# Optimization experiments

Hardware: AMD Instinct MI355X
Metric: run time of the kernel (lower is better)

## Reference

```python
import jax, jax.numpy as jnp
import numpy as np

N = 100000
E = 1600000
D_IN = 64
D_HID = 64
D_OUT = 40
BN_EPS = 1e-5


def setup_inputs() -> dict:
    key = jax.random.key(0)
    ks = jax.random.split(key, 8)
    x = jax.random.normal(ks[0], (N, D_IN), dtype=jnp.float32)
    edge_index = jax.random.randint(ks[1], (2, E), 0, N, dtype=jnp.int64)
    # SAGEConv params: out = lin_l(aggr_neigh) + lin_r(x); bias lives in lin_l
    s1 = 1.0 / np.sqrt(D_IN)
    W1l = jax.random.uniform(ks[2], (D_HID, D_IN), jnp.float32, -s1, s1)
    W1r = jax.random.uniform(ks[3], (D_HID, D_IN), jnp.float32, -s1, s1)
    b1 = jnp.zeros((D_HID,), jnp.float32)
    gamma = jnp.ones((D_HID,), jnp.float32)
    beta = jnp.zeros((D_HID,), jnp.float32)
    s2 = 1.0 / np.sqrt(D_HID)
    W2l = jax.random.uniform(ks[4], (D_OUT, D_HID), jnp.float32, -s2, s2)
    W2r = jax.random.uniform(ks[5], (D_OUT, D_HID), jnp.float32, -s2, s2)
    b2 = jnp.zeros((D_OUT,), jnp.float32)
    return {"x": x, "edge_index": edge_index, "W1l": W1l, "W1r": W1r, "b1": b1,
            "gamma": gamma, "beta": beta, "W2l": W2l, "W2r": W2r, "b2": b2}


def _scatter_mean(feat, src, dst, n):
    # gather source-node features, scatter-mean onto destination nodes
    summed = jax.ops.segment_sum(feat[src], dst, num_segments=n)  # [N, D]
    cnt = jax.ops.segment_sum(jnp.ones((src.shape[0],), feat.dtype), dst, num_segments=n)
    return summed / jnp.maximum(cnt, 1.0)[:, None]


def _sage_conv(h, src, dst, Wl, Wr, b):
    agg = _scatter_mean(h, src, dst, h.shape[0])
    return agg @ Wl.T + h @ Wr.T + b


def reference(x, edge_index, W1l, W1r, b1, gamma, beta, W2l, W2r, b2):
    src, dst = edge_index[0], edge_index[1]
    h = _sage_conv(x, src, dst, W1l, W1r, b1)
    # BatchNorm1d (training-mode batch statistics, biased variance)
    mu = jnp.mean(h, axis=0)
    var = jnp.mean(jnp.square(h - mu), axis=0)
    h = (h - mu) * jax.lax.rsqrt(var + BN_EPS) * gamma + beta
    h = jax.nn.relu(h)
    # dropout is identity in eval mode
    out = _sage_conv(h, src, dst, W2l, W2r, b2)
    return out
```

## Files before the change

### kernel.cpp

```cpp
#include <hip/hip_runtime.h>
#include <hip/hip_fp8.h>

#define N_NODES 100000
#define N_EDGES 1600000
#define BN_EPS 1e-5f
#define E4 400000
#define CAP 64
#define NBINS 391
#define BINCAP 4608
#define BIN_MASK 255
#define G_BLOCKS 6250
#define NCOPY 32
#define D1B 391

typedef float v2f __attribute__((ext_vector_type(2)));
typedef __attribute__((ext_vector_type(8))) short bf16x8;
typedef __attribute__((ext_vector_type(4))) float f32x4;

__device__ __forceinline__ float bcast(float v, int k) {
    return __uint_as_float(__builtin_amdgcn_readlane(__float_as_uint(v), k));
}
__device__ __forceinline__ unsigned short f2bf(float x) {
    unsigned int u = __float_as_uint(x);
    return (unsigned short)((u + 0x7FFF + ((u >> 16) & 1)) >> 16);
}
__device__ __forceinline__ bf16x8 pack8(float4 a, float4 b) {
    bf16x8 r;
    r[0] = (short)f2bf(a.x); r[1] = (short)f2bf(a.y);
    r[2] = (short)f2bf(a.z); r[3] = (short)f2bf(a.w);
    r[4] = (short)f2bf(b.x); r[5] = (short)f2bf(b.y);
    r[6] = (short)f2bf(b.z); r[7] = (short)f2bf(b.w);
    return r;
}
__device__ __forceinline__ unsigned char f2fp8(float x) {
    return (unsigned char)__hip_cvt_float_to_fp8(x, __HIP_SATFINITE, __HIP_E4M3);
}
template <bool HI>
__device__ __forceinline__ v2f fp8x2(unsigned int w) {
#if __has_builtin(__builtin_amdgcn_cvt_pk_f32_fp8)
    return __builtin_amdgcn_cvt_pk_f32_fp8((int)w, HI);
#else
    unsigned int b = HI ? (w >> 16) : w;
    __half_raw h0 = __hip_cvt_fp8_to_halfraw((__hip_fp8_storage_t)(b & 0xFF), __HIP_E4M3);
    __half_raw h1 = __hip_cvt_fp8_to_halfraw((__hip_fp8_storage_t)((b >> 8) & 0xFF), __HIP_E4M3);
    v2f r; r.x = __half2float(__half(h0)); r.y = __half2float(__half(h1));
    return r;
#endif
}

__global__ __launch_bounds__(1024) void binA_kernel(
    const int4* __restrict__ src4, const int4* __restrict__ dst4,
    int* __restrict__ bcur, unsigned int* __restrict__ binbuf)
{
    __shared__ int lcnt[NBINS];
    __shared__ int lbase[NBINS];
    int tid = threadIdx.x;
    if (tid < NBINS) lcnt[tid] = 0;
    __syncthreads();

    int i = blockIdx.x * 1024 + tid;
    int4 d, s;
    int b0 = 0, b1 = 0, b2 = 0, b3 = 0, r0 = 0, r1 = 0, r2 = 0, r3 = 0;
    bool valid = (i < E4);
    if (valid) {
        d = dst4[i]; s = src4[i];
        b0 = d.x >> 8; r0 = atomicAdd(&lcnt[b0], 1);
        b1 = d.y >> 8; r1 = atomicAdd(&lcnt[b1], 1);
        b2 = d.z >> 8; r2 = atomicAdd(&lcnt[b2], 1);
        b3 = d.w >> 8; r3 = atomicAdd(&lcnt[b3], 1);
    }
    __syncthreads();
    if (tid < NBINS && lcnt[tid] > 0)
        lbase[tid] = atomicAdd(&bcur[tid], lcnt[tid]);
    __syncthreads();
    if (valid) {
        int p;
        p = lbase[b0] + r0; if (p < BINCAP) binbuf[(size_t)b0 * BINCAP + p] = ((unsigned)s.x << 8) | (unsigned)(d.x & BIN_MASK);
        p = lbase[b1] + r1; if (p < BINCAP) binbuf[(size_t)b1 * BINCAP + p] = ((unsigned)s.y << 8) | (unsigned)(d.y & BIN_MASK);
        p = lbase[b2] + r2; if (p < BINCAP) binbuf[(size_t)b2 * BINCAP + p] = ((unsigned)s.z << 8) | (unsigned)(d.z & BIN_MASK);
        p = lbase[b3] + r3; if (p < BINCAP) binbuf[(size_t)b3 * BINCAP + p] = ((unsigned)s.w << 8) | (unsigned)(d.w & BIN_MASK);
    }
}

__global__ __launch_bounds__(256) void binB_dense1_kernel(
    const unsigned int* __restrict__ binbuf, const int* __restrict__ bcur,
    int* __restrict__ cnt, int* __restrict__ nbrf,
    const float* __restrict__ x, const float* __restrict__ W1l,
    const float* __restrict__ W1r, const float* __restrict__ b1,
    unsigned char* __restrict__ u8, float* __restrict__ hv)
{
    if (blockIdx.x < NBINS) {
        __shared__ int lc[256];
        int tid = threadIdx.x;
        lc[tid] = 0;
        __syncthreads();
        int bin = blockIdx.x;
        int n = min(bcur[bin], BINCAP);
        for (int i = tid; i < n; i += 256) {
            unsigned int e = binbuf[(size_t)bin * BINCAP + i];
            int dl  = (int)(e & BIN_MASK);
            int src = (int)(e >> 8);
            int slot = atomicAdd(&lc[dl], 1);
            if (slot < CAP)
                nbrf[((size_t)(bin * 256 + dl)) * CAP + slot] = src;
        }
        __syncthreads();
        int node = bin * 256 + tid;
        if (node < N_NODES) {
            int c = min(lc[tid], CAP);
            cnt[node] = c;
            if (c == 0) nbrf[(size_t)node * CAP] = 0;
        }
        return;
    }

    int lane = threadIdx.x & 63;
    int wv   = threadIdx.x >> 6;
    int lr   = lane & 15;
    int lk   = lane >> 4;

    bf16x8 Bf[2][4][2];
#pragma unroll
    for (int mat = 0; mat < 2; ++mat) {
        const float* W = mat ? W1r : W1l;
#pragma unroll
        for (int ft = 0; ft < 4; ++ft) {
#pragma unroll
            for (int kh = 0; kh < 2; ++kh) {
                const float* p = W + (size_t)(ft * 16 + lr) * 64 + kh * 32 + lk * 8;
                Bf[mat][ft][kh] = pack8(*(const float4*)p, *(const float4*)(p + 4));
            }
        }
    }
    float b1v[4];
#pragma unroll
    for (int ft = 0; ft < 4; ++ft) b1v[ft] = b1[ft * 16 + lr];

    int nb = (blockIdx.x - NBINS) * 256;

    for (int it = 0; it < 4; ++it) {
        int n0 = nb + it * 64 + wv * 16;
        int arow = min(n0 + lr, N_NODES - 1);
        const float* xp = x + (size_t)arow * 64 + lk * 8;
        bf16x8 a0 = pack8(*(const float4*)xp,        *(const float4*)(xp + 4));
        bf16x8 a1 = pack8(*(const float4*)(xp + 32), *(const float4*)(xp + 36));

#pragma unroll
        for (int ft = 0; ft < 4; ++ft) {
            f32x4 Cl = {0.f, 0.f, 0.f, 0.f};
            f32x4 Cr = {0.f, 0.f, 0.f, 0.f};
            Cl = __builtin_amdgcn_mfma_f32_16x16x32_bf16(a0, Bf[0][ft][0], Cl, 0, 0, 0);
            Cl = __builtin_amdgcn_mfma_f32_16x16x32_bf16(a1, Bf[0][ft][1], Cl, 0, 0, 0);
            Cr = __builtin_amdgcn_mfma_f32_16x16x32_bf16(a0, Bf[1][ft][0], Cr, 0, 0, 0);
            Cr = __builtin_amdgcn_mfma_f32_16x16x32_bf16(a1, Bf[1][ft][1], Cr, 0, 0, 0);
#pragma unroll
            for (int r = 0; r < 4; ++r) {
                int node = n0 + lk * 4 + r;
                if (node < N_NODES) {
                    u8[(size_t)node * 64 + ft * 16 + lr] = f2fp8(Cl[r]);
                    hv[(size_t)node * 64 + ft * 16 + lr] = Cr[r] + b1v[ft];
                }
            }
        }
    }
}

__global__ __launch_bounds__(256) void gather1_bn_kernel(
    const unsigned short* __restrict__ u16, const int* __restrict__ cnt,
    const int* __restrict__ nbrf, float* __restrict__ hv,
    float* __restrict__ sumsR)
{
    __shared__ int sdeg[16];
    int node0 = blockIdx.x * 16;
    if (threadIdx.x < 16) {
        int n = node0 + threadIdx.x;
        sdeg[threadIdx.x] = (n < N_NODES) ? min(cnt[n], CAP) : 0;
    }
    __syncthreads();

    int lane = threadIdx.x & 63;
    int m    = lane & 31;
    int half = lane >> 5;
    int wv   = threadIdx.x >> 6;
    float s1_0 = 0.f, s1_1 = 0.f, s2_0 = 0.f, s2_1 = 0.f;

    int d0  = sdeg[wv];
    int idn = nbrf[(size_t)min(node0 + wv, N_NODES - 1) * CAP + min(lane, max(d0, 1) - 1)];

    for (int nn = 0; nn < 4; ++nn) {
        int li   = nn * 4 + wv;
        int node = node0 + li;
        int deg  = sdeg[li];
        int id   = idn;

        if (nn < 3) {
            int lin = li + 4;
            int dn  = sdeg[lin];
            idn = nbrf[(size_t)min(node0 + lin, N_NODES - 1) * CAP + min(lane, max(dn, 1) - 1)];
        }

        if (node < N_NODES) {
            float2 v = make_float2(0.f, 0.f);
            if (half == 0)
                v = ((const float2*)hv)[(size_t)node * 32 + m];

            float p0=0,p1=0,p2=0,p3=0,q0=0,q1=0,q2=0,q3=0;
            for (int r = 0; r < deg; r += 16) {
#pragma unroll
                for (int i = 0; i < 8; ++i) {
                    int e   = r + 2 * i + half;
                    int ide = __shfl(id, e);
                    unsigned int w = u16[(size_t)ide * 32 + m];
                    w = (e < deg) ? w : 0u;
                    v2f d = fp8x2<false>(w);
                    if ((i & 3) == 0)      { p0 += d.x; q0 += d.y; }
                    else if ((i & 3) == 1) { p1 += d.x; q1 += d.y; }
                    else if ((i & 3) == 2) { p2 += d.x; q2 += d.y; }
                    else                   { p3 += d.x; q3 += d.y; }
                }
            }
            float P = (p0 + p1) + (p2 + p3);
            float Q = (q0 + q1) + (q2 + q3);
            P += __shfl_xor(P, 32);
            Q += __shfl_xor(Q, 32);
            if (half == 0) {
                float inv = 1.0f / (float)max(deg, 1);
                float h0 = P * inv + v.x;
                float h1 = Q * inv + v.y;
                ((float2*)hv)[(size_t)node * 32 + m] = make_float2(h0, h1);
                s1_0 += h0; s1_1 += h1;
                s2_0 += h0 * h0; s2_1 += h1 * h1;
            }
        }
    }

    __shared__ float2 redA[256];
    __shared__ float2 redB[256];
    redA[threadIdx.x] = make_float2(s1_0, s1_1);
    redB[threadIdx.x] = make_float2(s2_0, s2_1);
    __syncthreads();
    if (threadIdx.x < 32) {
        int mm = threadIdx.x;
        float a0=0,a1=0,b0=0,b1=0;
        for (int w = 0; w < 4; ++w) {
            float2 A = redA[w * 64 + mm]; a0 += A.x; a1 += A.y;
            float2 B = redB[w * 64 + mm]; b0 += B.x; b1 += B.y;
        }
        float* base = sumsR + (size_t)(blockIdx.x & (NCOPY - 1)) * 128;
        atomicAdd(&base[2 * mm], a0);       atomicAdd(&base[2 * mm + 1], a1);
        atomicAdd(&base[64 + 2 * mm], b0);  atomicAdd(&base[64 + 2 * mm + 1], b1);
    }
}

__global__ __launch_bounds__(256) void dense2_bn_kernel(
    const float* __restrict__ h, const float* __restrict__ sumsR,
    const float* __restrict__ gamma, const float* __restrict__ beta,
    const float* __restrict__ W2l, const float* __restrict__ W2r,
    const float* __restrict__ b2,
    unsigned char* __restrict__ t40, float* __restrict__ out)
{
    __shared__ float wlT[64 * 65];
    __shared__ float wrT[64 * 65];
    for (int idx = threadIdx.x; idx < 2560; idx += 256) {
        int f = idx >> 6, k = idx & 63;
        wlT[k * 65 + f] = W2l[idx];
        wrT[k * 65 + f] = W2r[idx];
    }
    __syncthreads();

    int f  = threadIdx.x & 63;
    int wv = threadIdx.x >> 6;
    int fc = (f < 40) ? f : 39;
    float wl[64], wr[64];
#pragma unroll
    for (int k = 0; k < 64; ++k) {
        wl[k] = wlT[k * 65 + fc];
        wr[k] = wrT[k * 65 + fc];
    }
    float bias = b2[fc];

    float s = 0.f, q = 0.f;
#pragma unroll
    for (int c = 0; c < NCOPY; ++c) {
        s += sumsR[c * 128 + f];
        q += sumsR[c * 128 + 64 + f];
    }
    float inv_n = 1.0f / (float)N_NODES;
    float mu  = s * inv_n;
    float var = q * inv_n - mu * mu;
    float rs  = rsqrtf(var + BN_EPS);
    float sc  = gamma[f] * rs;
    float sh  = beta[f] - mu * sc;

    int node0 = blockIdx.x * 64;

    for (int nn = 0; nn < 16; ++nn) {
        int node = node0 + nn * 4 + wv;
        if (node < N_NODES) {
            float hvv = h[(size_t)node * 64 + f];
            float hn  = fmaxf(hvv * sc + sh, 0.f);
            float ta = 0.f, ra = bias;
#pragma unroll
            for (int k = 0; k < 64; ++k) {
                float hb = bcast(hn, k);
                ta += hb * wl[k];
                ra += hb * wr[k];
            }
            if (f < 40) {
                t40[(size_t)node * 64 + f] = f2fp8(ta);
                out[(size_t)node * 40 + f] = ra;
            }
        }
    }
}

__global__ __launch_bounds__(256) void gather2_kernel(
    const unsigned int* __restrict__ t40, const int* __restrict__ cnt,
    const int* __restrict__ nbrf, float* __restrict__ out)
{
    __shared__ int sdeg[16];
    int node0 = blockIdx.x * 16;
    if (threadIdx.x < 16) {
        int n = node0 + threadIdx.x;
        sdeg[threadIdx.x] = (n < N_NODES) ? min(cnt[n], CAP) : 0;
    }
    __syncthreads();

    int lane = threadIdx.x & 63;
    int q    = lane >> 4;
    int m    = lane & 15;
    int cl   = (m < 10) ? m : 9;
    int wv   = threadIdx.x >> 6;

    int dA = sdeg[wv], dB = sdeg[wv + 4];
    int idA = nbrf[(size_t)min(node0 + wv,     N_NODES - 1) * CAP + min(lane, max(dA, 1) - 1)];
    int idB = nbrf[(size_t)min(node0 + wv + 4, N_NODES - 1) * CAP + min(lane, max(dB, 1) - 1)];

    unsigned int r0A[4], r1A[4], r0B[4], r1B[4];
    {
        int cnt0 = dA;
#pragma unroll
        for (int i = 0; i < 4; ++i) {
            int e   = 4 * i + q;
            int ide = __shfl(idA, max(min(e, cnt0 - 1), 0));
            r0A[i] = t40[(size_t)ide * 16 + cl];
        }
        if (cnt0 > 16) {
#pragma unroll
            for (int i = 0; i < 4; ++i) {
                int e   = 16 + 4 * i + q;
                int ide = __shfl(idA, min(e, cnt0 - 1));
                r1A[i] = t40[(size_t)ide * 16 + cl];
            }
        }
    }

    for (int nn = 0; nn < 4; ++nn) {
        int li   = nn * 4 + wv;
        int node = node0 + li;
        int deg  = sdeg[li];

        int idC = 0;
        if (nn < 2) {
            int lic = li + 8;
            int dc  = sdeg[lic];
            idC = nbrf[(size_t)min(node0 + lic, N_NODES - 1) * CAP + min(lane, max(dc, 1) - 1)];
        }
        if (nn < 3) {
            int cntn = sdeg[li + 4];
#pragma unroll
            for (int i = 0; i < 4; ++i) {
                int e   = 4 * i + q;
                int ide = __shfl(idB, max(min(e, cntn - 1), 0));
                r0B[i] = t40[(size_t)ide * 16 + cl];
            }
            if (cntn > 16) {
#pragma unroll
                for (int i = 0; i < 4; ++i) {
                    int e   = 16 + 4 * i + q;
                    int ide = __shfl(idB, min(e, cntn - 1));
                    r1B[i] = t40[(size_t)ide * 16 + cl];
                }
            }
        }

        if (node < N_NODES) {
            float4 o = make_float4(0.f, 0.f, 0.f, 0.f);
            if (lane < 10)
                o = ((const float4*)out)[(size_t)node * 10 + m];

            float a0=0,a1=0,a2=0,a3=0, b0=0,b1=0,b2=0,b3=0;
#pragma unroll
            for (int i = 0; i < 4; ++i) {
                int e = 4 * i + q;
                unsigned int w = (e < deg) ? r0A[i] : 0u;
                v2f dlo = fp8x2<false>(w);
                v2f dhi = fp8x2<true>(w);
                if (i & 1) { b0 += dlo.x; b1 += dlo.y; b2 += dhi.x; b3 += dhi.y; }
                else       { a0 += dlo.x; a1 += dlo.y; a2 += dhi.x; a3 += dhi.y; }
            }
            if (deg > 16) {
#pragma unroll
                for (int i = 0; i < 4; ++i) {
                    int e = 16 + 4 * i + q;
                    unsigned int w = (e < deg) ? r1A[i] : 0u;
                    v2f dlo = fp8x2<false>(w);
                    v2f dhi = fp8x2<true>(w);
                    if (i & 1) { b0 += dlo.x; b1 += dlo.y; b2 += dhi.x; b3 += dhi.y; }
                    else       { a0 += dlo.x; a1 += dlo.y; a2 += dhi.x; a3 += dhi.y; }
                }
                for (int r = 32; r < deg; r += 16) {
#pragma unroll
                    for (int i = 0; i < 4; ++i) {
                        int e   = r + 4 * i + q;
                        int ide = __shfl(idA, min(e, deg - 1));
                        unsigned int w = t40[(size_t)ide * 16 + cl];
                        w = (e < deg) ? w : 0u;
                        v2f dlo = fp8x2<false>(w);
                        v2f dhi = fp8x2<true>(w);
                        if (i & 1) { b0 += dlo.x; b1 += dlo.y; b2 += dhi.x; b3 += dhi.y; }
                        else       { a0 += dlo.x; a1 += dlo.y; a2 += dhi.x; a3 += dhi.y; }
                    }
                }
            }
            a0 += b0; a1 += b1; a2 += b2; a3 += b3;
            a0 += __shfl_xor(a0, 16); a0 += __shfl_xor(a0, 32);
            a1 += __shfl_xor(a1, 16); a1 += __shfl_xor(a1, 32);
            a2 += __shfl_xor(a2, 16); a2 += __shfl_xor(a2, 32);
            a3 += __shfl_xor(a3, 16); a3 += __shfl_xor(a3, 32);
            if (lane < 10) {
                float inv = 1.0f / (float)max(deg, 1);
                o.x += a0 * inv;
                o.y += a1 * inv;
                o.z += a2 * inv;
                o.w += a3 * inv;
                ((float4*)out)[(size_t)node * 10 + m] = o;
            }
        }

        idA = idB; idB = idC;
#pragma unroll
        for (int i = 0; i < 4; ++i) { r0A[i] = r0B[i]; r1A[i] = r1B[i]; }
    }
}

extern "C" void kernel_launch(void* const* d_in, const int* in_sizes, int n_in,
                              void* d_out, int out_size, void* d_ws, size_t ws_size,
                              hipStream_t stream)
{
    const float* x     = (const float*)d_in[0];
    const int*   ei    = (const int*)d_in[1];
    const float* W1l   = (const float*)d_in[2];
    const float* W1r   = (const float*)d_in[3];
    const float* b1    = (const float*)d_in[4];
    const float* gamma = (const float*)d_in[5];
    const float* beta  = (const float*)d_in[6];
    const float* W2l   = (const float*)d_in[7];
    const float* W2r   = (const float*)d_in[8];
    const float* b2    = (const float*)d_in[9];
    float* out = (float*)d_out;

    const int4* src4 = (const int4*)ei;
    const int4* dst4 = (const int4*)(ei + N_EDGES);

    float* ws    = (float*)d_ws;
    float* hv    = ws;
    float* sumsR = hv + (size_t)N_NODES * 64;
    int* bcur = (int*)(sumsR + NCOPY * 128);
    int* cnt  = bcur + 392;
    int* nbrf = cnt + N_NODES;
    unsigned char* u8 = (unsigned char*)(nbrf + (size_t)N_NODES * 64);
    unsigned char* t40 = u8;
    unsigned int* binbuf = (unsigned int*)d_out;

    dim3 blk(256);

    (void)hipMemsetAsync(sumsR, 0, (size_t)(NCOPY * 128 + 392) * 4, stream);

    int dblocks = (N_NODES + 63) / 64;

    binA_kernel<<<391, 1024, 0, stream>>>(src4, dst4, bcur, binbuf);

    binB_dense1_kernel<<<NBINS + D1B, blk, 0, stream>>>(
        binbuf, bcur, cnt, nbrf, x, W1l, W1r, b1, u8, hv);

    gather1_bn_kernel<<<G_BLOCKS, blk, 0, stream>>>(
        (const unsigned short*)u8, cnt, nbrf, hv, sumsR);

    dense2_bn_kernel<<<dblocks, blk, 0, stream>>>(
        hv, sumsR, gamma, beta, W2l, W2r, b2, t40, out);
    gather2_kernel<<<G_BLOCKS, blk, 0, stream>>>(
        (const unsigned int*)t40, cnt, nbrf, out);
}
```

Measured before the change: 265.0 us.

## Compute second-layer dense transform with bf16 MFMA instead of scalar FMA loops

Replaces the per-lane readlane-broadcast scalar FMA matmul in the BN+dense2 kernel with bf16 16x16x32 MFMA instructions, keeping the weights in registers as bf16 fragments. BN scale and shift are computed once per block into shared memory, and each block now processes 256 nodes with 391 blocks. The goal is to remove the heavy VALU and readlane cost of the 64x40 matmuls. In exchange, activations and weights are rounded to bf16 before the products, which lowers precision, and the output stores become strided per MFMA row layout.

Result: faster. 225.2 us (-15.0%).

```diff
diff --git a/kernel.cpp b/kernel.cpp
--- a/kernel.cpp
+++ b/kernel.cpp
@@ -259,56 +259,98 @@
     const float* __restrict__ b2,
     unsigned char* __restrict__ t40, float* __restrict__ out)
 {
-    __shared__ float wlT[64 * 65];
-    __shared__ float wrT[64 * 65];
-    for (int idx = threadIdx.x; idx < 2560; idx += 256) {
-        int f = idx >> 6, k = idx & 63;
-        wlT[k * 65 + f] = W2l[idx];
-        wrT[k * 65 + f] = W2r[idx];
-    }
-    __syncthreads();
-
-    int f  = threadIdx.x & 63;
-    int wv = threadIdx.x >> 6;
-    int fc = (f < 40) ? f : 39;
-    float wl[64], wr[64];
-#pragma unroll
-    for (int k = 0; k < 64; ++k) {
-        wl[k] = wlT[k * 65 + fc];
-        wr[k] = wrT[k * 65 + fc];
-    }
-    float bias = b2[fc];
-
-    float s = 0.f, q = 0.f;
-#pragma unroll
-    for (int c = 0; c < NCOPY; ++c) {
-        s += sumsR[c * 128 + f];
-        q += sumsR[c * 128 + 64 + f];
-    }
-    float inv_n = 1.0f / (float)N_NODES;
-    float mu  = s * inv_n;
-    float var = q * inv_n - mu * mu;
-    float rs  = rsqrtf(var + BN_EPS);
-    float sc  = gamma[f] * rs;
-    float sh  = beta[f] - mu * sc;
-
-    int node0 = blockIdx.x * 64;
-
-    for (int nn = 0; nn < 16; ++nn) {
-        int node = node0 + nn * 4 + wv;
-        if (node < N_NODES) {
-            float hvv = h[(size_t)node * 64 + f];
-            float hn  = fmaxf(hvv * sc + sh, 0.f);
-            float ta = 0.f, ra = bias;
-#pragma unroll
-            for (int k = 0; k < 64; ++k) {
-                float hb = bcast(hn, k);
-                ta += hb * wl[k];
-                ra += hb * wr[k];
-            }
-            if (f < 40) {
-                t40[(size_t)node * 64 + f] = f2fp8(ta);
-                out[(size_t)node * 40 + f] = ra;
+    __shared__ float ssc[64];
+    __shared__ float ssh[64];
+    if (threadIdx.x < 64) {
+        int f = threadIdx.x;
+        float s = 0.f, q = 0.f;
+#pragma unroll
+        for (int c = 0; c < NCOPY; ++c) {
+            s += sumsR[c * 128 + f];
+            q += sumsR[c * 128 + 64 + f];
+        }
+        float inv_n = 1.0f / (float)N_NODES;
+        float mu  = s * inv_n;
+        float var = q * inv_n - mu * mu;
+        float rs  = rsqrtf(var + BN_EPS);
+        float sc  = gamma[f] * rs;
+        ssc[f] = sc;
+        ssh[f] = beta[f] - mu * sc;
+    }
+    __syncthreads();
+
+    int lane = threadIdx.x & 63;
+    int wv   = threadIdx.x >> 6;
+    int lr   = lane & 15;
+    int lk   = lane >> 4;
+
+    float scA[8], shA[8], scB[8], shB[8];
+#pragma unroll
+    for (int j = 0; j < 8; ++j) {
+        scA[j] = ssc[lk * 8 + j];      shA[j] = ssh[lk * 8 + j];
+        scB[j] = ssc[32 + lk * 8 + j]; shB[j] = ssh[32 + lk * 8 + j];
+    }
+
+    bf16x8 Bt[3][2], Bo[3][2];
+#pragma unroll
+    for (int ft = 0; ft < 3; ++ft) {
+        int row = min(ft * 16 + lr, 39);
+#pragma unroll
+        for (int kh = 0; kh < 2; ++kh) {
+            const float* pl = W2l + (size_t)row * 64 + kh * 32 + lk * 8;
+            const float* pr = W2r + (size_t)row * 64 + kh * 32 + lk * 8;
+            Bt[ft][kh] = pack8(*(const float4*)pl, *(const float4*)(pl + 4));
+            Bo[ft][kh] = pack8(*(const float4*)pr, *(const float4*)(pr + 4));
+        }
+    }
+    float b2v[3];
+#pragma unroll
+    for (int ft = 0; ft < 3; ++ft) b2v[ft] = b2[min(ft * 16 + lr, 39)];
+
+    int nb = blockIdx.x * 256;
+
+    for (int it = 0; it < 4; ++it) {
+        int n0 = nb + it * 64 + wv * 16;
+        int arow = min(n0 + lr, N_NODES - 1);
+        const float* hp = h + (size_t)arow * 64 + lk * 8;
+        float4 h0a = *(const float4*)hp,        h0b = *(const float4*)(hp + 4);
+        float4 h1a = *(const float4*)(hp + 32), h1b = *(const float4*)(hp + 36);
+        float4 n0a, n0b, n1a, n1b;
+        n0a.x = fmaxf(h0a.x * scA[0] + shA[0], 0.f);
+        n0a.y = fmaxf(h0a.y * scA[1] + shA[1], 0.f);
+        n0a.z = fmaxf(h0a.z * scA[2] + shA[2], 0.f);
+        n0a.w = fmaxf(h0a.w * scA[3] + shA[3], 0.f);
+        n0b.x = fmaxf(h0b.x * scA[4] + shA[4], 0.f);
+        n0b.y = fmaxf(h0b.y * scA[5] + shA[5], 0.f);
+        n0b.z = fmaxf(h0b.z * scA[6] + shA[6], 0.f);
+        n0b.w = fmaxf(h0b.w * scA[7] + shA[7], 0.f);
+        n1a.x = fmaxf(h1a.x * scB[0] + shB[0], 0.f);
+        n1a.y = fmaxf(h1a.y * scB[1] + shB[1], 0.f);
+        n1a.z = fmaxf(h1a.z * scB[2] + shB[2], 0.f);
+        n1a.w = fmaxf(h1a.w * scB[3] + shB[3], 0.f);
+        n1b.x = fmaxf(h1b.x * scB[4] + shB[4], 0.f);
+        n1b.y = fmaxf(h1b.y * scB[5] + shB[5], 0.f);
+        n1b.z = fmaxf(h1b.z * scB[6] + shB[6], 0.f);
+        n1b.w = fmaxf(h1b.w * scB[7] + shB[7], 0.f);
+        bf16x8 a0 = pack8(n0a, n0b);
+        bf16x8 a1 = pack8(n1a, n1b);
+
+#pragma unroll
+        for (int ft = 0; ft < 3; ++ft) {
+            f32x4 Ct = {0.f, 0.f, 0.f, 0.f};
+            f32x4 Co = {0.f, 0.f, 0.f, 0.f};
+            Ct = __builtin_amdgcn_mfma_f32_16x16x32_bf16(a0, Bt[ft][0], Ct, 0, 0, 0);
+            Ct = __builtin_amdgcn_mfma_f32_16x16x32_bf16(a1, Bt[ft][1], Ct, 0, 0, 0);
+            Co = __builtin_amdgcn_mfma_f32_16x16x32_bf16(a0, Bo[ft][0], Co, 0, 0, 0);
+            Co = __builtin_amdgcn_mfma_f32_16x16x32_bf16(a1, Bo[ft][1], Co, 0, 0, 0);
+            int f = ft * 16 + lr;
+#pragma unroll
+            for (int r = 0; r < 4; ++r) {
+                int node = n0 + lk * 4 + r;
+                if (node < N_NODES && f < 40) {
+                    t40[(size_t)node * 64 + f] = f2fp8(Ct[r]);
+                    out[(size_t)node * 40 + f] = Co[r] + b2v[ft];
+                }
             }
         }
     }
@@ -477,8 +519,6 @@
 
     (void)hipMemsetAsync(sumsR, 0, (size_t)(NCOPY * 128 + 392) * 4, stream);
 
-    int dblocks = (N_NODES + 63) / 64;
-
     binA_kernel<<<391, 1024, 0, stream>>>(src4, dst4, bcur, binbuf);
 
     binB_dense1_kernel<<<NBINS + D1B, blk, 0, stream>>>(
@@ -487,7 +527,7 @@
     gather1_bn_kernel<<<G_BLOCKS, blk, 0, stream>>>(
         (const unsigned short*)u8, cnt, nbrf, hv, sumsR);
 
-    dense2_bn_kernel<<<dblocks, blk, 0, stream>>>(
+    dense2_bn_kernel<<<D1B, blk, 0, stream>>>(
         hv, sumsR, gamma, beta, W2l, W2r, b2, t40, out);
     gather2_kernel<<<G_BLOCKS, blk, 0, stream>>>(
         (const unsigned int*)t40, cnt, nbrf, out);
```
